# Kernel tuning notes

Measured on AMD Instinct MI355X. Metric: run time of the kernel, lower is better.

Reference implementation:

```python
import jax, jax.numpy as jnp
import numpy as np

B, N = 4, 1024
DIM, DEPTH, HEADS, DHEAD, MLP = 512, 6, 8, 64, 2048
INNER = HEADS * DHEAD
SCALE = DHEAD ** -0.5
EPS = 1e-5


def setup_inputs() -> dict:
    key = jax.random.key(0)
    ks = jax.random.split(key, 16)
    w = lambda k, shape: (jax.random.normal(k, shape, jnp.float32) * 0.02)
    D = DEPTH
    return {
        "g": jax.random.normal(ks[0], (B, N, DIM), jnp.float32),
        "x": jax.random.normal(ks[1], (B, N, DIM), jnp.float32),
        # PreNorm + SelfAttention
        "ln1_s": jnp.ones((D, DIM)), "ln1_b": jnp.zeros((D, DIM)),
        "Wqkv": w(ks[2], (D, DIM, 3 * INNER)),
        "Wo_sa": w(ks[3], (D, INNER, DIM)), "bo_sa": jnp.zeros((D, DIM)),
        # RelationalCrossAttention
        "lng_s": jnp.ones((D, DIM)), "lng_b": jnp.zeros((D, DIM)),
        "lnx_s": jnp.ones((D, DIM)), "lnx_b": jnp.zeros((D, DIM)),
        "Wq": w(ks[4], (D, DIM, INNER)),
        "Wk": w(ks[5], (D, DIM, INNER)),
        "Wv": w(ks[6], (D, DIM, INNER)), "bv": jnp.zeros((D, INNER)),
        "Wo_ca": w(ks[7], (D, INNER, DIM)), "bo_ca": jnp.zeros((D, DIM)),
        # PreNorm + FeedForward (same module applied twice per layer)
        "lnf_s": jnp.ones((D, DIM)), "lnf_b": jnp.zeros((D, DIM)),
        "W1": w(ks[8], (D, DIM, MLP)), "b1": jnp.zeros((D, MLP)),
        "W2": w(ks[9], (D, MLP, DIM)), "b2": jnp.zeros((D, DIM)),
    }


def _ln(t, s, b):
    m = t.mean(-1, keepdims=True)
    v = ((t - m) ** 2).mean(-1, keepdims=True)
    return (t - m) / jnp.sqrt(v + EPS) * s + b


def _split_heads(t):  # [b, n, h*d] -> [b, h, n, d]
    b, n, _ = t.shape
    return t.reshape(b, n, HEADS, DHEAD).transpose(0, 2, 1, 3)


def _merge_heads(t):  # [b, h, n, d] -> [b, n, h*d]
    b, h, n, d = t.shape
    return t.transpose(0, 2, 1, 3).reshape(b, n, h * d)


def _attend(q, k, v):
    dots = jnp.einsum('bhnd,bhmd->bhnm', q, k) * SCALE
    attn = jax.nn.softmax(jnp.nan_to_num(dots, nan=-jnp.inf), axis=-1)
    attn = jnp.nan_to_num(attn)  # nan_to_num(0.0) post-softmax as in source
    return jnp.einsum('bhnm,bhmd->bhnd', attn, jnp.nan_to_num(v))


def reference(g, x, ln1_s, ln1_b, Wqkv, Wo_sa, bo_sa, lng_s, lng_b, lnx_s, lnx_b,
              Wq, Wk, Wv, bv, Wo_ca, bo_ca, lnf_s, lnf_b, W1, b1, W2, b2):
    for i in range(DEPTH):
        def ff(t):
            h = jax.nn.gelu(_ln(t, lnf_s[i], lnf_b[i]) @ W1[i] + b1[i], approximate=False)
            return h @ W2[i] + b2[i]
        # relational cross attention: q,k from g, v from x
        gn = _ln(g, lng_s[i], lng_b[i])
        xn = _ln(x, lnx_s[i], lnx_b[i])
        q = _split_heads(gn @ Wq[i])
        k = _split_heads(gn @ Wk[i])
        v = _split_heads(xn @ Wv[i] + bv[i])
        x = _merge_heads(_attend(q, k, v)) @ Wo_ca[i] + bo_ca[i] + x
        x = ff(x) + x
        # pre-norm self attention (skip connection enabled)
        sn = _ln(x, ln1_s[i], ln1_b[i])
        qkv = sn @ Wqkv[i]
        qs, ks_, vs = jnp.split(qkv, 3, axis=-1)
        sa = _merge_heads(_attend(_split_heads(qs), _split_heads(ks_), _split_heads(vs)))
        x = sa @ Wo_sa[i] + bo_sa[i] + x
        x = ff(x) + x
    return x
```

## Files before the change

kernel.cpp:

```cpp
#include <hip/hip_runtime.h>
#include <hip/hip_bf16.h>
#include <cstdint>
#include <cstddef>

#define DEV __device__ __forceinline__

using f32x4 = __attribute__((ext_vector_type(4))) float;
using bfx8  = __attribute__((ext_vector_type(8))) __bf16;
using s16x8 = __attribute__((ext_vector_type(8))) short;

DEV uint16_t f2bf(float f) {
    union { float f; uint32_t u; } x; x.f = f;
    uint32_t r = x.u + 0x7fffu + ((x.u >> 16) & 1u);
    return (uint16_t)(r >> 16);
}

DEV float gelu_exact(float v) {
    return 0.5f * v * (1.0f + erff(v * 0.70710678118654752f));
}

DEV f32x4 mfma16(s16x8 a, s16x8 b, f32x4 c) {
    return __builtin_amdgcn_mfma_f32_16x16x32_bf16(
        __builtin_bit_cast(bfx8, a), __builtin_bit_cast(bfx8, b), c, 0, 0, 0);
}

DEV void async_lds16(const void* g, void* l) {
    __builtin_amdgcn_global_load_lds(
        (const __attribute__((address_space(1))) uint32_t*)g,
        (__attribute__((address_space(3))) uint32_t*)l, 16, 0, 0);
}

DEV void ln_row(const float* __restrict__ in, const float* __restrict__ sc,
                const float* __restrict__ bi, uint16_t* __restrict__ out, size_t row)
{
    const int lane = threadIdx.x & 63;
    const float* p = in + row * 512 + lane * 8;
    float4 a = *(const float4*)p;
    float4 b4 = *(const float4*)(p + 4);
    float v[8] = {a.x, a.y, a.z, a.w, b4.x, b4.y, b4.z, b4.w};
    float s = 0.f, sq = 0.f;
#pragma unroll
    for (int j = 0; j < 8; ++j) { s += v[j]; sq += v[j] * v[j]; }
#pragma unroll
    for (int o = 1; o < 64; o <<= 1) { s += __shfl_xor(s, o); sq += __shfl_xor(sq, o); }
    const float mean = s * (1.0f / 512.0f);
    const float var  = sq * (1.0f / 512.0f) - mean * mean;
    const float rstd = rsqrtf(var + 1e-5f);
    const int c = lane * 8;
    uint16_t o8[8];
#pragma unroll
    for (int j = 0; j < 8; ++j)
        o8[j] = f2bf((v[j] - mean) * rstd * sc[c + j] + bi[c + j]);
    uint4 pk;
    pk.x = (uint32_t)o8[0] | ((uint32_t)o8[1] << 16);
    pk.y = (uint32_t)o8[2] | ((uint32_t)o8[3] << 16);
    pk.z = (uint32_t)o8[4] | ((uint32_t)o8[5] << 16);
    pk.w = (uint32_t)o8[6] | ((uint32_t)o8[7] << 16);
    *reinterpret_cast<uint4*>(out + row * 512 + c) = pk;
}

__global__ __launch_bounds__(256)
void ln_bf16(const float* __restrict__ in, const float* __restrict__ sc,
             const float* __restrict__ bi, uint16_t* __restrict__ out)
{
    ln_row(in, sc, bi, out, (size_t)blockIdx.x * 4 + (threadIdx.x >> 6));
}

__global__ __launch_bounds__(256)
void ln2_bf16(const float* __restrict__ in0, const float* __restrict__ sc0,
              const float* __restrict__ bi0, uint16_t* __restrict__ out0,
              const float* __restrict__ in1, const float* __restrict__ sc1,
              const float* __restrict__ bi1, uint16_t* __restrict__ out1)
{
    const int sel = blockIdx.x >> 10;
    const size_t row = (size_t)(blockIdx.x & 1023) * 4 + (threadIdx.x >> 6);
    if (sel == 0) ln_row(in0, sc0, bi0, out0, row);
    else          ln_row(in1, sc1, bi1, out1, row);
}

__global__ __launch_bounds__(256)
void wtrans(const float* __restrict__ W, uint16_t* __restrict__ WT, int K, int N,
            size_t lstride, int row0)
{
    __shared__ float tile[32][33];
    const int l = blockIdx.z;
    const int k0 = blockIdx.x * 32, n0 = blockIdx.y * 32;
    const float* Wl = W + (size_t)l * K * N;
    uint16_t* WTl = WT + (size_t)l * lstride;
    const int tx = threadIdx.x, ty = threadIdx.y;
#pragma unroll
    for (int j = 0; j < 4; ++j)
        tile[ty + j * 8][tx] = Wl[(size_t)(k0 + ty + j * 8) * N + n0 + tx];
    __syncthreads();
#pragma unroll
    for (int j = 0; j < 4; ++j)
        WTl[(size_t)(row0 + n0 + ty + j * 8) * K + k0 + tx] = f2bf(tile[tx][ty + j * 8]);
}

__global__ __launch_bounds__(256)
void vtrans(const uint16_t* __restrict__ src, uint16_t* __restrict__ vt, int C, int coff)
{
    __shared__ uint16_t tile[64][72];
    const int n0 = blockIdx.x * 64;
    const int bh = blockIdx.y, b = bh >> 3, h = bh & 7;
    const int tx = threadIdx.x, ty = threadIdx.y;
#pragma unroll
    for (int j = 0; j < 16; ++j) {
        const int n = ty + j * 4;
        tile[n][tx] = src[((size_t)b * 1024 + n0 + n) * C + coff + h * 64 + tx];
    }
    __syncthreads();
    uint16_t* o = vt + (size_t)bh * 65536;
#pragma unroll
    for (int j = 0; j < 16; ++j) {
        const int d = ty + j * 4;
        o[(size_t)d * 1024 + n0 + tx] = tile[tx][d];
    }
}

template<int BM, int BN, int NWR, int NWC, int HAS_BIAS, int HAS_RESID, int DO_GELU, int OUT_BF16>
__global__ __launch_bounds__(512, 4)
void gemm2(const uint16_t* __restrict__ A, const uint16_t* __restrict__ BT,
           const float* __restrict__ bias, const float* __restrict__ resid,
           void* __restrict__ outp, int M, int N, int K)
{
    constexpr int WM = BM / NWR, WN = BN / NWC;
    constexpr int FM = WM / 16, FN = WN / 16;
    constexpr int ASLOTS = 8 * BM, BSLOTS = 8 * BN, TOT = ASLOTS + BSLOTS;
    __shared__ uint16_t As[2][ASLOTS * 8];
    __shared__ uint16_t Bs[2][BSLOTS * 8];
    const int tid = threadIdx.x, lane = tid & 63;
    const int w = tid >> 6, wr = w / NWC, wc = w % NWC;
    const int kg = lane >> 4, lr = lane & 15;
    const int nbx = M / BM;
    const int id = blockIdx.x;
    const size_t m0 = (size_t)(id % nbx) * BM;
    const size_t n0 = (size_t)(id / nbx) * BN;

    auto stage = [&](int b, int k0) {
#pragma unroll
        for (int j = 0; j < TOT / 512; ++j) {
            const int s = j * 512 + tid;
            if (s < ASLOTS) {
                const int sub = s / BM, row = s % BM;
                async_lds16(A + (m0 + row) * K + k0 + sub * 8, &As[b][s * 8]);
            } else {
                const int s2 = s - ASLOTS;
                const int sub = s2 / BN, row = s2 % BN;
                async_lds16(BT + (n0 + row) * K + k0 + sub * 8, &Bs[b][s2 * 8]);
            }
        }
    };

    f32x4 acc[FM][FN] = {};
    const int nt = K / 64;
    stage(0, 0);
    __syncthreads();
    int cur = 0;
    for (int t = 0; t < nt; ++t) {
        if (t + 1 < nt) stage(cur ^ 1, (t + 1) * 64);
        s16x8 af[2][FM], bf[2][FN];
#pragma unroll
        for (int ks = 0; ks < 2; ++ks) {
#pragma unroll
            for (int i = 0; i < FM; ++i)
                af[ks][i] = *(const s16x8*)&As[cur][((ks * 4 + kg) * BM + wr * WM + i * 16 + lr) * 8];
#pragma unroll
            for (int j = 0; j < FN; ++j)
                bf[ks][j] = *(const s16x8*)&Bs[cur][((ks * 4 + kg) * BN + wc * WN + j * 16 + lr) * 8];
        }
        __builtin_amdgcn_s_setprio(1);
#pragma unroll
        for (int ks = 0; ks < 2; ++ks)
#pragma unroll
            for (int i = 0; i < FM; ++i)
#pragma unroll
                for (int j = 0; j < FN; ++j)
                    acc[i][j] = mfma16(af[ks][i], bf[ks][j], acc[i][j]);
        __builtin_amdgcn_s_setprio(0);
        __syncthreads();
        cur ^= 1;
    }
#pragma unroll
    for (int i = 0; i < FM; ++i) {
        const size_t rbase = m0 + wr * WM + i * 16 + kg * 4;
#pragma unroll
        for (int j = 0; j < FN; ++j) {
            const size_t col = n0 + wc * WN + j * 16 + lr;
            const float bval = HAS_BIAS ? bias[col] : 0.0f;
#pragma unroll
            for (int r = 0; r < 4; ++r) {
                const size_t row = rbase + r;
                float v = acc[i][j][r] + bval;
                if (DO_GELU)  v = gelu_exact(v);
                if (HAS_RESID) v += resid[row * (size_t)N + col];
                if (OUT_BF16) ((uint16_t*)outp)[row * (size_t)N + col] = f2bf(v);
                else          ((float*)outp)[row * (size_t)N + col] = v;
            }
        }
    }
}

__global__ __launch_bounds__(256)
void attn_flash(const uint16_t* __restrict__ Qb, const uint16_t* __restrict__ Kb,
                const uint16_t* __restrict__ Vt, uint16_t* __restrict__ Ob,
                int qstride, int kstride, int qoff, int koff)
{
    __shared__ uint16_t Ks[2][4096];
    __shared__ uint16_t Vs[2][4096];
    __shared__ uint16_t Pb[4][1024];
    const int tid = threadIdx.x, lane = tid & 63, w = tid >> 6;
    const int kg = lane >> 4, lr = lane & 15;
    const int bh = blockIdx.y, b = bh >> 3, h = bh & 7;
    const int q0 = blockIdx.x * 64;
    const float CEXP = 0.125f * 1.44269504f;

    s16x8 aq0, aq1;
    {
        const size_t qrow = (size_t)b * 1024 + q0 + w * 16 + lr;
        const uint16_t* qp = Qb + qrow * qstride + qoff + h * 64 + kg * 8;
        aq0 = *(const s16x8*)qp;
        aq1 = *(const s16x8*)(qp + 32);
    }
    const uint16_t* kbase = Kb + (size_t)b * 1024 * kstride + koff + h * 64;
    const uint16_t* vbase = Vt + (size_t)bh * 65536;

    float l_r[4] = {0.f, 0.f, 0.f, 0.f};
    f32x4 acc[4] = {};

    auto stage = [&](int buf, int kv0) {
#pragma unroll
        for (int j = 0; j < 2; ++j) {
            const int s = j * 256 + tid;
            const int sub = s >> 6, row = s & 63;
            async_lds16(kbase + (size_t)(kv0 + row) * kstride + sub * 8, &Ks[buf][s * 8]);
            async_lds16(vbase + (size_t)row * 1024 + kv0 + sub * 8,      &Vs[buf][s * 8]);
        }
    };

    stage(0, 0);
    __syncthreads();
    int cur = 0;
    for (int t = 0; t < 16; ++t) {
        if (t < 15) stage(cur ^ 1, (t + 1) * 64);
        f32x4 s4[4];
        __builtin_amdgcn_s_setprio(1);
#pragma unroll
        for (int ni = 0; ni < 4; ++ni) {
            s16x8 bk0 = *(const s16x8*)&Ks[cur][(kg * 64 + ni * 16 + lr) * 8];
            s16x8 bk1 = *(const s16x8*)&Ks[cur][((4 + kg) * 64 + ni * 16 + lr) * 8];
            f32x4 z = {};
            z = mfma16(aq0, bk0, z);
            z = mfma16(aq1, bk1, z);
            s4[ni] = z;
        }
        __builtin_amdgcn_s_setprio(0);
#pragma unroll
        for (int ni = 0; ni < 4; ++ni) {
            const int slotb = (ni * 2 + (lr >> 3)) * 16 + kg * 4;
#pragma unroll
            for (int r = 0; r < 4; ++r) {
                const float pe = __builtin_amdgcn_exp2f(s4[ni][r] * CEXP);
                l_r[r] += pe;
                Pb[w][(slotb + r) * 8 + (lr & 7)] = f2bf(pe);
            }
        }
        s16x8 ap0 = *(const s16x8*)&Pb[w][(kg * 16 + lr) * 8];
        s16x8 ap1 = *(const s16x8*)&Pb[w][((4 + kg) * 16 + lr) * 8];
        __builtin_amdgcn_s_setprio(1);
#pragma unroll
        for (int ni = 0; ni < 4; ++ni) {
            s16x8 bv0 = *(const s16x8*)&Vs[cur][(kg * 64 + ni * 16 + lr) * 8];
            s16x8 bv1 = *(const s16x8*)&Vs[cur][((4 + kg) * 64 + ni * 16 + lr) * 8];
            acc[ni] = mfma16(ap0, bv0, acc[ni]);
            acc[ni] = mfma16(ap1, bv1, acc[ni]);
        }
        __builtin_amdgcn_s_setprio(0);
        __syncthreads();
        cur ^= 1;
    }
    float linv[4];
#pragma unroll
    for (int r = 0; r < 4; ++r) {
        float l = l_r[r];
        l += __shfl_xor(l, 1); l += __shfl_xor(l, 2);
        l += __shfl_xor(l, 4); l += __shfl_xor(l, 8);
        linv[r] = 1.0f / l;
    }
#pragma unroll
    for (int ni = 0; ni < 4; ++ni)
#pragma unroll
        for (int r = 0; r < 4; ++r) {
            const float v = acc[ni][r] * linv[r];
            const size_t row = (size_t)b * 1024 + q0 + w * 16 + kg * 4 + r;
            Ob[row * 512 + h * 64 + ni * 16 + lr] = f2bf(v);
        }
}

extern "C" void kernel_launch(void* const* d_in, const int* in_sizes, int n_in,
                              void* d_out, int out_size, void* d_ws, size_t ws_size,
                              hipStream_t stream)
{
    (void)in_sizes; (void)n_in; (void)out_size; (void)ws_size;
    const float* g     = (const float*)d_in[0];
    const float* x0    = (const float*)d_in[1];
    const float* ln1_s = (const float*)d_in[2];
    const float* ln1_b = (const float*)d_in[3];
    const float* Wqkv  = (const float*)d_in[4];
    const float* Wo_sa = (const float*)d_in[5];
    const float* bo_sa = (const float*)d_in[6];
    const float* lng_s = (const float*)d_in[7];
    const float* lng_b = (const float*)d_in[8];
    const float* lnx_s = (const float*)d_in[9];
    const float* lnx_b = (const float*)d_in[10];
    const float* Wq    = (const float*)d_in[11];
    const float* Wk    = (const float*)d_in[12];
    const float* Wv    = (const float*)d_in[13];
    const float* bv    = (const float*)d_in[14];
    const float* Wo_ca = (const float*)d_in[15];
    const float* bo_ca = (const float*)d_in[16];
    const float* lnf_s = (const float*)d_in[17];
    const float* lnf_b = (const float*)d_in[18];
    const float* W1    = (const float*)d_in[19];
    const float* b1    = (const float*)d_in[20];
    const float* W2    = (const float*)d_in[21];
    const float* b2    = (const float*)d_in[22];

    float* x = (float*)d_out;

    char* p = (char*)d_ws;
    auto carve = [&](size_t n) { char* r = p; p += (n + 255) & ~(size_t)255; return r; };
    uint16_t* WqkT  = (uint16_t*)carve(6ull * 1024 * 512 * 2);
    uint16_t* WvT   = (uint16_t*)carve(6ull * 512 * 512 * 2);
    uint16_t* WocaT = (uint16_t*)carve(6ull * 512 * 512 * 2);
    uint16_t* WqkvT = (uint16_t*)carve(6ull * 1536 * 512 * 2);
    uint16_t* WosaT = (uint16_t*)carve(6ull * 512 * 512 * 2);
    uint16_t* W1T   = (uint16_t*)carve(6ull * 2048 * 512 * 2);
    uint16_t* W2T   = (uint16_t*)carve(6ull * 512 * 2048 * 2);
    uint16_t* gn    = (uint16_t*)carve(4096ull * 512 * 2);
    uint16_t* xn    = (uint16_t*)carve(4096ull * 512 * 2);
    uint16_t* qkvu  = (uint16_t*)carve(4096ull * 1536 * 2);
    uint16_t* vt    = (uint16_t*)carve(32ull * 64 * 1024 * 2);
    uint16_t* ab    = (uint16_t*)carve(4096ull * 512 * 2);
    uint16_t* hb    = (uint16_t*)carve(4096ull * 2048 * 2);
    uint16_t* qk = qkvu;
    uint16_t* vb = qkvu + 4096ull * 1024;

    dim3 tb(32, 8);
    wtrans<<<dim3(16, 16, 6), tb, 0, stream>>>(Wq,    WqkT,  512, 512,  1024ull * 512, 0);
    wtrans<<<dim3(16, 16, 6), tb, 0, stream>>>(Wk,    WqkT,  512, 512,  1024ull * 512, 512);
    wtrans<<<dim3(16, 16, 6), tb, 0, stream>>>(Wv,    WvT,   512, 512,  512ull * 512, 0);
    wtrans<<<dim3(16, 16, 6), tb, 0, stream>>>(Wo_ca, WocaT, 512, 512,  512ull * 512, 0);
    wtrans<<<dim3(16, 48, 6), tb, 0, stream>>>(Wqkv,  WqkvT, 512, 1536, 1536ull * 512, 0);
    wtrans<<<dim3(16, 16, 6), tb, 0, stream>>>(Wo_sa, WosaT, 512, 512,  512ull * 512, 0);
    wtrans<<<dim3(16, 64, 6), tb, 0, stream>>>(W1,    W1T,   512, 2048, 2048ull * 512, 0);
    wtrans<<<dim3(64, 16, 6), tb, 0, stream>>>(W2,    W2T,   2048, 512, 2048ull * 512, 0);

    hipMemcpyAsync(x, x0, 4096ull * 512 * 4, hipMemcpyDeviceToDevice, stream);

    const dim3 ga(16, 32), va(16, 32), vb4(64, 4);

    for (int l = 0; l < 6; ++l) {
        const size_t o512 = (size_t)l * 512, oW = (size_t)l * 512 * 512;
        const size_t oW1 = (size_t)l * 2048 * 512, oWqkv = (size_t)l * 1536 * 512;
        const size_t o2048 = (size_t)l * 2048;

        ln2_bf16<<<2048, 256, 0, stream>>>(g, lng_s + o512, lng_b + o512, gn,
                                           x, lnx_s + o512, lnx_b + o512, xn);
        gemm2<128, 128, 2, 4, 0, 0, 0, 1><<<256, 512, 0, stream>>>(
            gn, WqkT + (size_t)l * 1024 * 512, nullptr, nullptr, qk, 4096, 1024, 512);
        gemm2<128, 64, 4, 2, 1, 0, 0, 1><<<256, 512, 0, stream>>>(
            xn, WvT + oW, bv + o512, nullptr, vb, 4096, 512, 512);
        vtrans<<<va, vb4, 0, stream>>>(vb, vt, 512, 0);
        attn_flash<<<ga, 256, 0, stream>>>(qk, qk, vt, ab, 1024, 1024, 0, 512);
        gemm2<128, 64, 4, 2, 1, 1, 0, 0><<<256, 512, 0, stream>>>(
            ab, WocaT + oW, bo_ca + o512, x, x, 4096, 512, 512);

        ln_bf16<<<1024, 256, 0, stream>>>(x, lnf_s + o512, lnf_b + o512, xn);
        gemm2<128, 128, 2, 4, 1, 0, 1, 1><<<512, 512, 0, stream>>>(
            xn, W1T + oW1, b1 + o2048, nullptr, hb, 4096, 2048, 512);
        gemm2<128, 64, 4, 2, 1, 1, 0, 0><<<256, 512, 0, stream>>>(
            hb, W2T + oW1, b2 + o512, x, x, 4096, 512, 2048);

        ln_bf16<<<1024, 256, 0, stream>>>(x, ln1_s + o512, ln1_b + o512, xn);
        gemm2<128, 128, 2, 4, 0, 0, 0, 1><<<384, 512, 0, stream>>>(
            xn, WqkvT + oWqkv, nullptr, nullptr, qkvu, 4096, 1536, 512);
        vtrans<<<va, vb4, 0, stream>>>(qkvu, vt, 1536, 1024);
        attn_flash<<<ga, 256, 0, stream>>>(qkvu, qkvu, vt, ab, 1536, 1536, 0, 512);
        gemm2<128, 64, 4, 2, 1, 1, 0, 0><<<256, 512, 0, stream>>>(
            ab, WosaT + oW, bo_sa + o512, x, x, 4096, 512, 512);

        ln_bf16<<<1024, 256, 0, stream>>>(x, lnf_s + o512, lnf_b + o512, xn);
        gemm2<128, 128, 2, 4, 1, 0, 1, 1><<<512, 512, 0, stream>>>(
            xn, W1T + oW1, b1 + o2048, nullptr, hb, 4096, 2048, 512);
        gemm2<128, 64, 4, 2, 1, 1, 0, 0><<<256, 512, 0, stream>>>(
            hb, W2T + oW1, b2 + o512, x, x, 4096, 512, 2048);
    }
}
```

Before: 1.679 ms.

## Deepen GEMM prefetch with explicit vmcnt waits and XCD-aware block remap

Reworks the GEMM main loop so two K-tiles are issued up front. Each iteration waits only on the older tile's async loads via explicit s_waitcnt vmcnt, and the next-next tile is issued after a raw barrier. This replaces the full __syncthreads drain with finer-grained waits so global loads overlap more MFMA work. It also remaps block IDs across the 8 XCDs and switches to row-major tile ordering to improve L2 locality. The hand-written waitcnt and barrier sequencing relies on exact load counts per thread, which is fragile if the stage loop or the compiler's scheduling changes.

After: 1.712 ms. Within noise of the previous version (+2.0%).

```diff
diff --git a/kernel.cpp b/kernel.cpp
--- a/kernel.cpp
+++ b/kernel.cpp
@@ -29,6 +29,16 @@
         (const __attribute__((address_space(1))) uint32_t*)g,
         (__attribute__((address_space(3))) uint32_t*)l, 16, 0, 0);
 }
+
+template<int N> DEV void wait_vmcnt() {
+    if constexpr (N == 0)      asm volatile("s_waitcnt vmcnt(0)" ::: "memory");
+    else if constexpr (N == 3) asm volatile("s_waitcnt vmcnt(3)" ::: "memory");
+    else if constexpr (N == 4) asm volatile("s_waitcnt vmcnt(4)" ::: "memory");
+    else static_assert(N == 0 || N == 3 || N == 4, "add vmcnt literal");
+}
+#define SBAR      asm volatile("s_barrier" ::: "memory")
+#define LGKM0     asm volatile("s_waitcnt lgkmcnt(0)" ::: "memory")
+#define SCHED0    __builtin_amdgcn_sched_barrier(0)
 
 DEV void ln_row(const float* __restrict__ in, const float* __restrict__ sc,
                 const float* __restrict__ bi, uint16_t* __restrict__ out, size_t row)
@@ -120,26 +130,29 @@
 
 template<int BM, int BN, int NWR, int NWC, int HAS_BIAS, int HAS_RESID, int DO_GELU, int OUT_BF16>
 __global__ __launch_bounds__(512, 4)
-void gemm2(const uint16_t* __restrict__ A, const uint16_t* __restrict__ BT,
+void gemm3(const uint16_t* __restrict__ A, const uint16_t* __restrict__ BT,
            const float* __restrict__ bias, const float* __restrict__ resid,
            void* __restrict__ outp, int M, int N, int K)
 {
     constexpr int WM = BM / NWR, WN = BN / NWC;
     constexpr int FM = WM / 16, FN = WN / 16;
     constexpr int ASLOTS = 8 * BM, BSLOTS = 8 * BN, TOT = ASLOTS + BSLOTS;
+    constexpr int S = TOT / 512;
     __shared__ uint16_t As[2][ASLOTS * 8];
     __shared__ uint16_t Bs[2][BSLOTS * 8];
     const int tid = threadIdx.x, lane = tid & 63;
     const int w = tid >> 6, wr = w / NWC, wc = w % NWC;
     const int kg = lane >> 4, lr = lane & 15;
-    const int nbx = M / BM;
-    const int id = blockIdx.x;
-    const size_t m0 = (size_t)(id % nbx) * BM;
-    const size_t n0 = (size_t)(id / nbx) * BN;
+    const int nwg = gridDim.x;
+    const int id0 = blockIdx.x;
+    const int id = (id0 & 7) * (nwg >> 3) + (id0 >> 3);
+    const int nbn = N / BN;
+    const size_t m0 = (size_t)(id / nbn) * BM;
+    const size_t n0 = (size_t)(id % nbn) * BN;
 
     auto stage = [&](int b, int k0) {
 #pragma unroll
-        for (int j = 0; j < TOT / 512; ++j) {
+        for (int j = 0; j < S; ++j) {
             const int s = j * 512 + tid;
             if (s < ASLOTS) {
                 const int sub = s / BM, row = s % BM;
@@ -155,10 +168,11 @@
     f32x4 acc[FM][FN] = {};
     const int nt = K / 64;
     stage(0, 0);
-    __syncthreads();
+    stage(1, 64);
     int cur = 0;
     for (int t = 0; t < nt; ++t) {
-        if (t + 1 < nt) stage(cur ^ 1, (t + 1) * 64);
+        if (t < nt - 1) wait_vmcnt<S>(); else wait_vmcnt<0>();
+        SBAR;
         s16x8 af[2][FM], bf[2][FN];
 #pragma unroll
         for (int ks = 0; ks < 2; ++ks) {
@@ -178,7 +192,9 @@
                 for (int j = 0; j < FN; ++j)
                     acc[i][j] = mfma16(af[ks][i], bf[ks][j], acc[i][j]);
         __builtin_amdgcn_s_setprio(0);
-        __syncthreads();
+        LGKM0; SCHED0;
+        SBAR;
+        if (t + 2 < nt) stage(cur, (t + 2) * 64);
         cur ^= 1;
     }
 #pragma unroll
@@ -367,33 +383,33 @@
 
         ln2_bf16<<<2048, 256, 0, stream>>>(g, lng_s + o512, lng_b + o512, gn,
                                            x, lnx_s + o512, lnx_b + o512, xn);
-        gemm2<128, 128, 2, 4, 0, 0, 0, 1><<<256, 512, 0, stream>>>(
+        gemm3<128, 128, 2, 4, 0, 0, 0, 1><<<256, 512, 0, stream>>>(
             gn, WqkT + (size_t)l * 1024 * 512, nullptr, nullptr, qk, 4096, 1024, 512);
-        gemm2<128, 64, 4, 2, 1, 0, 0, 1><<<256, 512, 0, stream>>>(
+        gemm3<128, 64, 4, 2, 1, 0, 0, 1><<<256, 512, 0, stream>>>(
             xn, WvT + oW, bv + o512, nullptr, vb, 4096, 512, 512);
         vtrans<<<va, vb4, 0, stream>>>(vb, vt, 512, 0);
         attn_flash<<<ga, 256, 0, stream>>>(qk, qk, vt, ab, 1024, 1024, 0, 512);
-        gemm2<128, 64, 4, 2, 1, 1, 0, 0><<<256, 512, 0, stream>>>(
+        gemm3<128, 64, 4, 2, 1, 1, 0, 0><<<256, 512, 0, stream>>>(
             ab, WocaT + oW, bo_ca + o512, x, x, 4096, 512, 512);
 
         ln_bf16<<<1024, 256, 0, stream>>>(x, lnf_s + o512, lnf_b + o512, xn);
-        gemm2<128, 128, 2, 4, 1, 0, 1, 1><<<512, 512, 0, stream>>>(
+        gemm3<128, 128, 2, 4, 1, 0, 1, 1><<<512, 512, 0, stream>>>(
             xn, W1T + oW1, b1 + o2048, nullptr, hb, 4096, 2048, 512);
-        gemm2<128, 64, 4, 2, 1, 1, 0, 0><<<256, 512, 0, stream>>>(
+        gemm3<128, 64, 4, 2, 1, 1, 0, 0><<<256, 512, 0, stream>>>(
             hb, W2T + oW1, b2 + o512, x, x, 4096, 512, 2048);
 
         ln_bf16<<<1024, 256, 0, stream>>>(x, ln1_s + o512, ln1_b + o512, xn);
-        gemm2<128, 128, 2, 4, 0, 0, 0, 1><<<384, 512, 0, stream>>>(
+        gemm3<128, 128, 2, 4, 0, 0, 0, 1><<<384, 512, 0, stream>>>(
             xn, WqkvT + oWqkv, nullptr, nullptr, qkvu, 4096, 1536, 512);
         vtrans<<<va, vb4, 0, stream>>>(qkvu, vt, 1536, 1024);
         attn_flash<<<ga, 256, 0, stream>>>(qkvu, qkvu, vt, ab, 1536, 1536, 0, 512);
-        gemm2<128, 64, 4, 2, 1, 1, 0, 0><<<256, 512, 0, stream>>>(
+        gemm3<128, 64, 4, 2, 1, 1, 0, 0><<<256, 512, 0, stream>>>(
             ab, WosaT + oW, bo_sa + o512, x, x, 4096, 512, 512);
 
         ln_bf16<<<1024, 256, 0, stream>>>(x, lnf_s + o512, lnf_b + o512, xn);
-        gemm2<128, 128, 2, 4, 1, 0, 1, 1><<<512, 512, 0, stream>>>(
+        gemm3<128, 128, 2, 4, 1, 0, 1, 1><<<512, 512, 0, stream>>>(
             xn, W1T + oW1, b1 + o2048, nullptr, hb, 4096, 2048, 512);
-        gemm2<128, 64, 4, 2, 1, 1, 0, 0><<<256, 512, 0, stream>>>(
+        gemm3<128, 64, 4, 2, 1, 1, 0, 0><<<256, 512, 0, stream>>>(
             hb, W2T + oW1, b2 + o512, x, x, 4096, 512, 2048);
     }
 }
```
